# Kernel tuning notes

Hardware: AMD Instinct MI355X
Metric: run time of the kernel (lower is better)

## Reference

```python
import jax, jax.numpy as jnp
import numpy as np
import math

B, L, D, H, FACTOR = 4, 2048, 256, 8, 5
DH = D // H

def setup_inputs() -> dict:
    key = jax.random.key(0)
    ks = jax.random.split(key, 12)
    s = 1.0 / math.sqrt(D)
    return {
        "q": jax.random.normal(ks[0], (B, L, D), jnp.float32),
        "k": jax.random.normal(ks[1], (B, L, D), jnp.float32),
        "v": jax.random.normal(ks[2], (B, L, D), jnp.float32),
        "Wq": jax.random.normal(ks[3], (D, D), jnp.float32) * s,
        "bq": jax.random.normal(ks[4], (D,), jnp.float32) * s,
        "Wk": jax.random.normal(ks[5], (D, D), jnp.float32) * s,
        "bk": jax.random.normal(ks[6], (D,), jnp.float32) * s,
        "Wv": jax.random.normal(ks[7], (D, D), jnp.float32) * s,
        "bv": jax.random.normal(ks[8], (D,), jnp.float32) * s,
        "Wc": jax.random.normal(ks[9], (D, D), jnp.float32) * s,
        "bc": jax.random.normal(ks[10], (D,), jnp.float32) * s,
        "index_sample": jax.random.randint(ks[11], (L,), 0, L),  # U_part = min(5*L*ceil(log1p(L)), L) = L
    }

def reference(q, k, v, Wq, bq, Wk, bk, Wv, bv, Wc, bc, index_sample):
    # projections (torch Linear: x @ W^T + b)
    qp = q @ Wq.T + bq
    kp = k @ Wk.T + bk
    vp = v @ Wv.T + bv
    # NOTE: original reshapes q with a raw view (no transpose), k/v via split()
    q4 = qp.reshape(B, H, L, DH)                       # faithful to q.view(B, H, L, dh)
    k4 = kp.reshape(B, L, H, DH).transpose(0, 2, 1, 3)
    v4 = vp.reshape(B, L, H, DH).transpose(0, 2, 1, 3)
    qf = q4.reshape(B * H, L, DH)
    kf = k4.reshape(B * H, L, DH)
    vf = v4.reshape(B * H, L, DH)
    # random K sampling (with replacement); U_part == L here
    K_sample = kf[:, index_sample, :]                  # [BH, L, dh]
    QK = jnp.einsum('bld,bud->blu', qf, K_sample)      # [BH, L, L]
    M = QK.max(axis=-1) - QK.sum(axis=-1) / L          # sparsity measure [BH, L]
    u = min(FACTOR * math.ceil(math.log1p(L)), L)      # = 40
    _, top_idx = jax.lax.top_k(-M, u)                  # topk(..., largest=False)
    Q_red = jnp.take_along_axis(qf, top_idx[:, :, None], axis=1)  # [BH, u, dh]
    scores = jnp.einsum('bud,bld->bul', Q_red, kf) / math.sqrt(DH)
    probs = jax.nn.softmax(scores, axis=-1)
    out = jnp.einsum('bul,bld->bud', probs, vf)        # [BH, u, dh]
    out = out.reshape(B, H, u, DH).transpose(0, 2, 1, 3).reshape(B, u, D)
    return out @ Wc.T + bc
```

## Files before the change

### kernel.cpp

```cpp
#include <hip/hip_runtime.h>
#include <math.h>

#define B_ 4
#define L_ 2048
#define D_ 256
#define H_ 8
#define DH_ 32
#define NH_ 32
#define U_ 40
#define LD_ 524288
#define NCH_ 16

typedef __attribute__((ext_vector_type(8))) short short8;
typedef __attribute__((ext_vector_type(4))) float floatx4;

static __device__ __forceinline__ unsigned long long ullmin_(unsigned long long a, unsigned long long b) {
    return a < b ? a : b;
}
static __device__ __forceinline__ unsigned short f2bf_rne(float x) {
    unsigned u = __float_as_uint(x);
    unsigned r = u + 0x7FFFu + ((u >> 16) & 1u);
    return (unsigned short)(r >> 16);
}
static __device__ __forceinline__ float bf2f(unsigned short h) {
    return __uint_as_float(((unsigned)h) << 16);
}

__global__ __launch_bounds__(256) void gemm_mfma3(const float* __restrict__ q,
                                                  const float* __restrict__ k,
                                                  const float* __restrict__ v,
                                                  const float* __restrict__ Wq,
                                                  const float* __restrict__ Wk,
                                                  const float* __restrict__ Wv,
                                                  const float* __restrict__ bq,
                                                  const float* __restrict__ bk,
                                                  const float* __restrict__ bv,
                                                  float* __restrict__ qp,
                                                  float* __restrict__ kp,
                                                  float* __restrict__ vp) {
    const int mat = blockIdx.z;
    const float* X = (mat == 0) ? q : (mat == 1) ? k : v;
    const float* W = (mat == 0) ? Wq : (mat == 1) ? Wk : Wv;
    const float* bias = (mat == 0) ? bq : (mat == 1) ? bk : bv;
    float* Y = (mat == 0) ? qp : (mat == 1) ? kp : vp;

    const int t = threadIdx.x;
    const int w = t >> 6, lane = t & 63;
    const int lq = lane & 15, quad = lane >> 4;
    const int colBase = blockIdx.y * 64;
    const int rowBaseW = blockIdx.x * 128 + w * 32;

    __shared__ unsigned short Bls[24576];

    floatx4 acc[2][4];
#pragma unroll
    for (int mt = 0; mt < 2; ++mt)
#pragma unroll
        for (int nt = 0; nt < 4; ++nt) acc[mt][nt] = (floatx4){0.f, 0.f, 0.f, 0.f};

    for (int phase = 0; phase < 2; ++phase) {
        __syncthreads();
#pragma unroll
        for (int r = 0; r < 8; ++r) {
            const int e = t + 256 * r;
            const int col = e >> 5;
            const int k4u = e & 31;
            const int kk = phase * 128 + k4u * 4;
            const float4 x = *(const float4*)(W + (size_t)(colBase + col) * 256 + kk);
            float xs[4] = {x.x, x.y, x.z, x.w};
            unsigned short hv[4], mv4[4], lv[4];
#pragma unroll
            for (int j = 0; j < 4; ++j) {
                hv[j] = f2bf_rne(xs[j]);
                const float e1 = xs[j] - bf2f(hv[j]);
                mv4[j] = f2bf_rne(e1);
                const float e2 = e1 - bf2f(mv4[j]);
                lv[j] = f2bf_rne(e2);
            }
            const int nt = col >> 4, cin = col & 15;
            const int ktl = k4u >> 3, kin = (k4u & 7) * 4;
            const int base = nt * 512 + cin * 32 + kin;
            *(ushort4*)&Bls[((0 * 4 + ktl) << 11) + base] = make_ushort4(hv[0], hv[1], hv[2], hv[3]);
            *(ushort4*)&Bls[((1 * 4 + ktl) << 11) + base] = make_ushort4(mv4[0], mv4[1], mv4[2], mv4[3]);
            *(ushort4*)&Bls[((2 * 4 + ktl) << 11) + base] = make_ushort4(lv[0], lv[1], lv[2], lv[3]);
        }
        __syncthreads();

#pragma unroll
        for (int ktl = 0; ktl < 4; ++ktl) {
            const int kt = phase * 4 + ktl;
            short8 Bh[4], Bm[4], Bl[4];
            const int fo = lq * 32 + quad * 8;
#pragma unroll
            for (int j = 0; j < 4; ++j) {
                Bh[j] = *(const short8*)&Bls[((0 * 4 + ktl) << 11) + j * 512 + fo];
                Bm[j] = *(const short8*)&Bls[((1 * 4 + ktl) << 11) + j * 512 + fo];
                Bl[j] = *(const short8*)&Bls[((2 * 4 + ktl) << 11) + j * 512 + fo];
            }
#pragma unroll
            for (int mt = 0; mt < 2; ++mt) {
                const int m = rowBaseW + mt * 16 + lq;
                short8 Ah, Am, Al;
                {
                    const float* xr = X + (size_t)m * 256 + kt * 32 + quad * 8;
                    const float4 x0 = *(const float4*)xr;
                    const float4 x1 = *(const float4*)(xr + 4);
                    float xs[8] = {x0.x, x0.y, x0.z, x0.w, x1.x, x1.y, x1.z, x1.w};
#pragma unroll
                    for (int j = 0; j < 8; ++j) {
                        const unsigned short h = f2bf_rne(xs[j]);
                        const float e1 = xs[j] - bf2f(h);
                        const unsigned short md = f2bf_rne(e1);
                        const float e2 = e1 - bf2f(md);
                        Ah[j] = (short)h;
                        Am[j] = (short)md;
                        Al[j] = (short)f2bf_rne(e2);
                    }
                }
#pragma unroll
                for (int j = 0; j < 4; ++j) {
                    floatx4 a = acc[mt][j];
                    a = __builtin_amdgcn_mfma_f32_16x16x32_bf16(Am, Bm[j], a, 0, 0, 0);
                    a = __builtin_amdgcn_mfma_f32_16x16x32_bf16(Ah, Bl[j], a, 0, 0, 0);
                    a = __builtin_amdgcn_mfma_f32_16x16x32_bf16(Al, Bh[j], a, 0, 0, 0);
                    a = __builtin_amdgcn_mfma_f32_16x16x32_bf16(Ah, Bm[j], a, 0, 0, 0);
                    a = __builtin_amdgcn_mfma_f32_16x16x32_bf16(Am, Bh[j], a, 0, 0, 0);
                    a = __builtin_amdgcn_mfma_f32_16x16x32_bf16(Ah, Bh[j], a, 0, 0, 0);
                    acc[mt][j] = a;
                }
            }
        }
    }

#pragma unroll
    for (int mt = 0; mt < 2; ++mt)
#pragma unroll
        for (int nt = 0; nt < 4; ++nt) {
            const int c = colBase + nt * 16 + lq;
            const float bv_ = bias[c];
#pragma unroll
            for (int r = 0; r < 4; ++r) {
                const int mr = rowBaseW + mt * 16 + quad * 4 + r;
                Y[(size_t)mr * 256 + c] = acc[mt][nt][r] + bv_;
            }
        }
}

__global__ __launch_bounds__(256) void gemm_out(const float* __restrict__ X,
                                                const float* __restrict__ Wc,
                                                const float* __restrict__ bias,
                                                float* __restrict__ Y) {
    const int t = threadIdx.x;
    const int rowBase = blockIdx.x * 16;
    const int colBase = blockIdx.y * 64;
    const int col = colBase + (t & 63);
    const int rq = (t >> 6) * 4;

    __shared__ float Xs[16][256];
#pragma unroll
    for (int e = t; e < 1024; e += 256) {
        const int r = e >> 6, kq = (e & 63) * 4;
        *(float4*)&Xs[r][kq] = *(const float4*)(X + (size_t)(rowBase + r) * 256 + kq);
    }
    __syncthreads();

    const float* wr = Wc + (size_t)col * 256;
    float acc[4] = {0.f, 0.f, 0.f, 0.f};
#pragma unroll 8
    for (int k = 0; k < 256; k += 4) {
        const float4 wv = *(const float4*)(wr + k);
#pragma unroll
        for (int r = 0; r < 4; ++r) {
            acc[r] = fmaf(Xs[rq + r][k + 0], wv.x, acc[r]);
            acc[r] = fmaf(Xs[rq + r][k + 1], wv.y, acc[r]);
            acc[r] = fmaf(Xs[rq + r][k + 2], wv.z, acc[r]);
            acc[r] = fmaf(Xs[rq + r][k + 3], wv.w, acc[r]);
        }
    }

    const float bv = bias[col];
#pragma unroll
    for (int r = 0; r < 4; ++r)
        Y[(size_t)(rowBase + rq + r) * 256 + col] = acc[r] + bv;
}

__global__ __launch_bounds__(256) void kconv_ksum(const float* __restrict__ kp,
                                                  const int* __restrict__ idx,
                                                  unsigned short* __restrict__ Khi,
                                                  unsigned short* __restrict__ Klo,
                                                  float* __restrict__ Ksum32) {
    const int blk = blockIdx.x;
    const int i = blk >> 5, uc = blk & 31;
    const int b = i >> 3, h = i & 7;
    const int t = threadIdx.x;
    const int dq = (t & 7) * 4;
    const int ur = t >> 3;

    __shared__ float part[32][36];
    float ksum[4] = {0.f, 0.f, 0.f, 0.f};

#pragma unroll
    for (int p = 0; p < 2; ++p) {
        int u = uc * 64 + p * 32 + ur;
        const float4 x = *(const float4*)(kp + (size_t)b * LD_ + (size_t)idx[u] * D_ + h * DH_ + dq);
        float xs[4] = {x.x, x.y, x.z, x.w};
        unsigned short hv[4], lv[4];
#pragma unroll
        for (int j = 0; j < 4; ++j) {
            ksum[j] += xs[j];
            hv[j] = f2bf_rne(xs[j]);
            lv[j] = f2bf_rne(xs[j] - bf2f(hv[j]));
        }
        size_t o = ((size_t)i * 2048 + u) * 32 + dq;
        *(ushort4*)(Khi + o) = make_ushort4(hv[0], hv[1], hv[2], hv[3]);
        *(ushort4*)(Klo + o) = make_ushort4(lv[0], lv[1], lv[2], lv[3]);
    }
#pragma unroll
    for (int j = 0; j < 4; ++j) part[ur][dq + j] = ksum[j];
    __syncthreads();
    if (t < 32) {
        float s = 0.f;
#pragma unroll 8
        for (int u2 = 0; u2 < 32; ++u2) s += part[u2][t];
        Ksum32[(size_t)blk * 32 + t] = s;
    }
}

__global__ __launch_bounds__(256) void mpart_mfma(const float* __restrict__ qp,
                                                  const unsigned short* __restrict__ Khi,
                                                  const unsigned short* __restrict__ Klo,
                                                  const float* __restrict__ Ksum32,
                                                  float* __restrict__ Mv,
                                                  float* __restrict__ Qmean) {
    const int blk = blockIdx.x;
    const int i = blk >> 5;
    const int lg = blk & 31;
    const int t = threadIdx.x;
    const int w = t >> 6;
    const int lane = t & 63;
    const int lq = lane & 15;
    const int quad = lane >> 4;

    __shared__ float ssum[32];
    __shared__ float red[4][64];
    if (t < 32) {
        float s = 0.f;
#pragma unroll 8
        for (int uc = 0; uc < 32; ++uc) s += Ksum32[((size_t)i * 32 + uc) * 32 + t];
        ssum[t] = s;
    }

    short8 Ah[4], Al[4];
#pragma unroll
    for (int lt = 0; lt < 4; ++lt) {
        const int l = lg * 64 + lt * 16 + lq;
        const float* qrow = qp + ((size_t)i * 2048 + l) * 32 + quad * 8;
        float4 x0 = *(const float4*)(qrow);
        float4 x1 = *(const float4*)(qrow + 4);
        float xs[8] = {x0.x, x0.y, x0.z, x0.w, x1.x, x1.y, x1.z, x1.w};
#pragma unroll
        for (int j = 0; j < 8; ++j) {
            unsigned short h = f2bf_rne(xs[j]);
            unsigned short lo = f2bf_rne(xs[j] - bf2f(h));
            Ah[lt][j] = (short)h;
            Al[lt][j] = (short)lo;
        }
    }

    floatx4 rmax[4];
#pragma unroll
    for (int lt = 0; lt < 4; ++lt)
        rmax[lt] = (floatx4){-INFINITY, -INFINITY, -INFINITY, -INFINITY};

    const size_t kfrag = ((size_t)i * 2048 + w * 512 + lq) * 32 + quad * 8;
    const unsigned short* ph = Khi + kfrag;
    const unsigned short* pl = Klo + kfrag;
#pragma unroll 2
    for (int s = 0; s < 32; ++s) {
        short8 Bh = *(const short8*)(ph + (size_t)s * 512);
        short8 Bl = *(const short8*)(pl + (size_t)s * 512);
#pragma unroll
        for (int lt = 0; lt < 4; ++lt) {
            floatx4 acc = (floatx4){0.f, 0.f, 0.f, 0.f};
            acc = __builtin_amdgcn_mfma_f32_16x16x32_bf16(Al[lt], Bh, acc, 0, 0, 0);
            acc = __builtin_amdgcn_mfma_f32_16x16x32_bf16(Ah[lt], Bl, acc, 0, 0, 0);
            acc = __builtin_amdgcn_mfma_f32_16x16x32_bf16(Ah[lt], Bh, acc, 0, 0, 0);
#pragma unroll
            for (int r = 0; r < 4; ++r) rmax[lt][r] = fmaxf(rmax[lt][r], acc[r]);
        }
    }

#pragma unroll
    for (int lt = 0; lt < 4; ++lt)
#pragma unroll
        for (int r = 0; r < 4; ++r) {
            float v = rmax[lt][r];
#pragma unroll
            for (int off = 1; off < 16; off <<= 1)
                v = fmaxf(v, __shfl_xor(v, off, 64));
            rmax[lt][r] = v;
        }
    if (lq == 0) {
#pragma unroll
        for (int lt = 0; lt < 4; ++lt)
#pragma unroll
            for (int r = 0; r < 4; ++r)
                red[w][lt * 16 + quad * 4 + r] = rmax[lt][r];
    }
    __syncthreads();
    if (t < 64) {
        const int l = lg * 64 + t;
        float m = fmaxf(fmaxf(red[0][t], red[1][t]), fmaxf(red[2][t], red[3][t]));
        const float4* q4 = (const float4*)(qp + ((size_t)i * 2048 + l) * 32);
        const float4* s4 = (const float4*)ssum;
        float qs = 0.f;
#pragma unroll
        for (int z = 0; z < 8; ++z) {
            float4 a = q4[z];
            float4 c = s4[z];
            qs = fmaf(a.x, c.x, qs);
            qs = fmaf(a.y, c.y, qs);
            qs = fmaf(a.z, c.z, qs);
            qs = fmaf(a.w, c.w, qs);
        }
        const float qm = qs * (1.0f / 2048.0f);
        Qmean[(size_t)i * 2048 + l] = qm;
        Mv[(size_t)i * 2048 + l] = m - qm;
    }
}

__global__ __launch_bounds__(256) void topk64_kernel(const float* __restrict__ Mv,
                                                     int* __restrict__ candIdx) {
    const int i = blockIdx.x;
    const int t = threadIdx.x;
    unsigned long long keys[8];
    __shared__ unsigned long long wred[4];
#pragma unroll
    for (int j = 0; j < 8; ++j) {
        const int l = t + 256 * j;
        unsigned u32 = __float_as_uint(Mv[(size_t)i * 2048 + l]);
        u32 = (u32 & 0x80000000u) ? ~u32 : (u32 | 0x80000000u);
        keys[j] = ((unsigned long long)u32 << 32) | (unsigned)l;
    }
    for (int it = 0; it < 64; ++it) {
        unsigned long long best = keys[0];
#pragma unroll
        for (int j = 1; j < 8; ++j) best = ullmin_(best, keys[j]);
#pragma unroll
        for (int off = 1; off < 64; off <<= 1)
            best = ullmin_(best, __shfl_xor(best, off, 64));
        if ((t & 63) == 0) wred[t >> 6] = best;
        __syncthreads();
        const unsigned long long m = ullmin_(ullmin_(wred[0], wred[1]), ullmin_(wred[2], wred[3]));
        if (t == 0) candIdx[i * 64 + it] = (int)(m & 0xffffffffu);
#pragma unroll
        for (int j = 0; j < 8; ++j)
            if (keys[j] == m) keys[j] = ~0ULL;
        __syncthreads();
    }
}

__global__ __launch_bounds__(256) void refine_kernel(const float* __restrict__ qp,
                                                     const float* __restrict__ kp,
                                                     const int* __restrict__ idx,
                                                     const int* __restrict__ candIdx,
                                                     float* __restrict__ refPart) {
    const int blk = blockIdx.x;
    const int i = blk >> 3, c = blk & 7;
    const int b = i >> 3, h = i & 7;
    const int t = threadIdx.x;
    __shared__ float qc[64][40];
    __shared__ float Ks[128][40];

    {
        const int cand = t >> 2, dp = (t & 3) * 8;
        const int l = candIdx[i * 64 + cand];
        const float* src = qp + ((size_t)i * 2048 + l) * 32 + dp;
        *(float4*)&qc[cand][dp] = *(const float4*)(src);
        *(float4*)&qc[cand][dp + 4] = *(const float4*)(src + 4);
    }
    __syncthreads();

    const int cand = t >> 2, usub = t & 3;
    float qv[32];
#pragma unroll
    for (int z = 0; z < 8; ++z) {
        float4 a = *(const float4*)&qc[cand][z * 4];
        qv[4 * z] = a.x; qv[4 * z + 1] = a.y; qv[4 * z + 2] = a.z; qv[4 * z + 3] = a.w;
    }

    float m = -INFINITY;
    for (int s = 0; s < 2; ++s) {
        {
            const int r = t >> 1, half = t & 1;
            const int u = c * 256 + s * 128 + r;
            const float* krow = kp + (size_t)b * LD_ + (size_t)idx[u] * D_ + h * DH_ + half * 16;
#pragma unroll
            for (int z = 0; z < 4; ++z)
                *(float4*)&Ks[r][half * 16 + z * 4] = *(const float4*)(krow + z * 4);
        }
        __syncthreads();
        for (int ur = usub; ur < 128; ur += 4) {
            float a0 = 0, a1 = 0, a2 = 0, a3 = 0;
#pragma unroll
            for (int z = 0; z < 8; ++z) {
                float4 kv = *(const float4*)&Ks[ur][z * 4];
                a0 = fmaf(qv[4 * z], kv.x, a0);
                a1 = fmaf(qv[4 * z + 1], kv.y, a1);
                a2 = fmaf(qv[4 * z + 2], kv.z, a2);
                a3 = fmaf(qv[4 * z + 3], kv.w, a3);
            }
            m = fmaxf(m, (a0 + a1) + (a2 + a3));
        }
        __syncthreads();
    }
    m = fmaxf(m, __shfl_xor(m, 1, 64));
    m = fmaxf(m, __shfl_xor(m, 2, 64));
    if ((t & 3) == 0) refPart[((size_t)i * 8 + c) * 64 + cand] = m;
}

__global__ __launch_bounds__(64) void select40_kernel(const int* __restrict__ candIdx,
                                                      const float* __restrict__ refPart,
                                                      const float* __restrict__ Qmean,
                                                      int* __restrict__ topIdx) {
    const int i = blockIdx.x;
    const int t = threadIdx.x;
    const int l = candIdx[i * 64 + t];
    float m = -INFINITY;
#pragma unroll
    for (int c = 0; c < 8; ++c) m = fmaxf(m, refPart[((size_t)i * 8 + c) * 64 + t]);
    float Mex = m - Qmean[(size_t)i * 2048 + l];
    unsigned u32 = __float_as_uint(Mex);
    u32 = (u32 & 0x80000000u) ? ~u32 : (u32 | 0x80000000u);
    unsigned long long key = ((unsigned long long)u32 << 32) | (unsigned)l;
    for (int it = 0; it < 40; ++it) {
        unsigned long long k2 = key;
#pragma unroll
        for (int off = 1; off < 64; off <<= 1) k2 = ullmin_(k2, __shfl_xor(k2, off, 64));
        if (key == k2) {
            topIdx[i * 40 + it] = l;
            key = ~0ULL;
        }
    }
}

#define SCP2 136
#define VSP 36

__global__ __launch_bounds__(320) void attn_part(const float* __restrict__ qp,
                                                 const float* __restrict__ kp,
                                                 const float* __restrict__ vp,
                                                 const int* __restrict__ topIdx,
                                                 float* __restrict__ mPart,
                                                 float* __restrict__ sPart,
                                                 float* __restrict__ oPart) {
    const int blk = blockIdx.x;
    const int i = blk >> 4, c = blk & 15;
    const int b = i >> 3, h = i & 7;
    const int t = threadIdx.x;

    __shared__ float Qs[40][32];
    __shared__ float Vs[128][VSP];
    __shared__ float sc[40][SCP2];
    __shared__ float mred[40], sred[40];

    {
        const int r = t >> 3, qq = t & 7;
        const int lq = topIdx[i * 40 + r];
        *(float4*)&Qs[r][qq * 4] = *(const float4*)(qp + ((size_t)i * 2048 + lq) * 32 + qq * 4);
    }
    for (int e = t; e < 1024; e += 320) {
        const int r = e >> 3, qq = e & 7;
        *(float4*)&Vs[r][qq * 4] =
            *(const float4*)(vp + (size_t)b * LD_ + (size_t)(c * 128 + r) * 256 + h * 32 + qq * 4);
    }
    __syncthreads();

    const float scale = 0.17677669529663687f;

    if (t < 256) {
        const int r = t >> 1;
        const int j0 = (t & 1) * 20;
        const float* kr = kp + (size_t)b * LD_ + (size_t)(c * 128 + r) * 256 + h * 32;
        float kv[32];
#pragma unroll
        for (int z = 0; z < 8; ++z) {
            float4 x = *(const float4*)(kr + z * 4);
            kv[4 * z] = x.x; kv[4 * z + 1] = x.y; kv[4 * z + 2] = x.z; kv[4 * z + 3] = x.w;
        }
#pragma unroll 4
        for (int jj = 0; jj < 20; ++jj) {
            const int j = j0 + jj;
            float a0 = 0, a1 = 0, a2 = 0, a3 = 0;
#pragma unroll
            for (int z = 0; z < 8; ++z) {
                const float4 q4 = *(const float4*)&Qs[j][z * 4];
                a0 = fmaf(kv[4 * z], q4.x, a0);
                a1 = fmaf(kv[4 * z + 1], q4.y, a1);
                a2 = fmaf(kv[4 * z + 2], q4.z, a2);
                a3 = fmaf(kv[4 * z + 3], q4.w, a3);
            }
            sc[j][r] = ((a0 + a1) + (a2 + a3)) * scale;
        }
    }
    __syncthreads();

    {
        const int w = t >> 6, lane = t & 63;
#pragma unroll
        for (int rr = 0; rr < 8; ++rr) {
            const int j = w * 8 + rr;
            float x0 = sc[j][lane], x1 = sc[j][lane + 64];
            float m = fmaxf(x0, x1);
#pragma unroll
            for (int off = 1; off < 64; off <<= 1) m = fmaxf(m, __shfl_xor(m, off, 64));
            const float e0 = __expf(x0 - m), e1 = __expf(x1 - m);
            sc[j][lane] = e0; sc[j][lane + 64] = e1;
            float s = e0 + e1;
#pragma unroll
            for (int off = 1; off < 64; off <<= 1) s += __shfl_xor(s, off, 64);
            if (lane == 0) { mred[j] = m; sred[j] = s; }
        }
    }
    __syncthreads();

    {
        const int j = t >> 3, qq = t & 7;
        float4 acc = make_float4(0.f, 0.f, 0.f, 0.f);
        for (int l = 0; l < 128; ++l) {
            const float p = sc[j][l];
            const float4 v4 = *(const float4*)&Vs[l][qq * 4];
            acc.x = fmaf(p, v4.x, acc.x);
            acc.y = fmaf(p, v4.y, acc.y);
            acc.z = fmaf(p, v4.z, acc.z);
            acc.w = fmaf(p, v4.w, acc.w);
        }
        const size_t o = (size_t)(i * NCH_ + c) * 40 + j;
        *(float4*)&oPart[o * 32 + qq * 4] = acc;
        if (qq == 0) { mPart[o] = mred[j]; sPart[o] = sred[j]; }
    }
}

__global__ __launch_bounds__(256) void attn_combine(const float* __restrict__ mPart,
                                                    const float* __restrict__ sPart,
                                                    const float* __restrict__ oPart,
                                                    float* __restrict__ attnOut) {
    const int i = blockIdx.x;
    const int b = i >> 3, h = i & 7;
    const int t = threadIdx.x;
    for (int e = t; e < 1280; e += 256) {
        const int j = e >> 5, d = e & 31;
        float mv[NCH_];
        float M = -INFINITY;
#pragma unroll
        for (int c = 0; c < NCH_; ++c) {
            mv[c] = mPart[(size_t)(i * NCH_ + c) * 40 + j];
            M = fmaxf(M, mv[c]);
        }
        float S = 0.f, O = 0.f;
#pragma unroll
        for (int c = 0; c < NCH_; ++c) {
            const float sc_ = __expf(mv[c] - M);
            const size_t o = (size_t)(i * NCH_ + c) * 40 + j;
            S = fmaf(sPart[o], sc_, S);
            O = fmaf(oPart[o * 32 + d], sc_, O);
        }
        attnOut[((size_t)b * 40 + j) * 256 + h * 32 + d] = O / S;
    }
}

extern "C" void kernel_launch(void* const* d_in, const int* in_sizes, int n_in,
                              void* d_out, int out_size, void* d_ws, size_t ws_size,
                              hipStream_t stream) {
    const float* q  = (const float*)d_in[0];
    const float* k  = (const float*)d_in[1];
    const float* v  = (const float*)d_in[2];
    const float* Wq = (const float*)d_in[3];
    const float* bq = (const float*)d_in[4];
    const float* Wk = (const float*)d_in[5];
    const float* bk = (const float*)d_in[6];
    const float* Wv = (const float*)d_in[7];
    const float* bv = (const float*)d_in[8];
    const float* Wc = (const float*)d_in[9];
    const float* bc = (const float*)d_in[10];
    const int* idx  = (const int*)d_in[11];
    float* out = (float*)d_out;

    char* w = (char*)d_ws;
    float*          qp      = (float*)(w);
    float*          kp      = (float*)(w + (8u << 20));
    float*          vp      = (float*)(w + (16u << 20));
    unsigned short* Khi     = (unsigned short*)(w + (24u << 20));
    unsigned short* Klo     = (unsigned short*)(w + (28u << 20));
    float*          Mv      = (float*)(w + (32u << 20));
    float*          Qmean   = (float*)(w + (32u << 20) + (256u << 10));
    float*          Ksum32  = (float*)(w + (32u << 20) + (512u << 10));
    int*            candIdx = (int*)  (w + (32u << 20) + (640u << 10));
    int*            topIdx  = (int*)  (w + (32u << 20) + (648u << 10));
    float*          refPart = (float*)(w + (32u << 20) + (656u << 10));
    float*          attnOut = (float*)(w + (32u << 20) + (720u << 10));
    float*          mPart   = (float*)(w + (24u << 20));
    float*          sPart   = (float*)(w + (24u << 20) + (128u << 10));
    float*          oPart   = (float*)(w + (24u << 20) + (256u << 10));

    hipLaunchKernelGGL(gemm_mfma3, dim3(64, 4, 3), dim3(256), 0, stream,
                       q, k, v, Wq, Wk, Wv, bq, bk, bv, qp, kp, vp);
    hipLaunchKernelGGL(kconv_ksum, dim3(1024), dim3(256), 0, stream, kp, idx, Khi, Klo, Ksum32);
    hipLaunchKernelGGL(mpart_mfma, dim3(1024), dim3(256), 0, stream, qp, Khi, Klo, Ksum32, Mv, Qmean);
    hipLaunchKernelGGL(topk64_kernel, dim3(32), dim3(256), 0, stream, Mv, candIdx);
    hipLaunchKernelGGL(refine_kernel, dim3(256), dim3(256), 0, stream, qp, kp, idx, candIdx, refPart);
    hipLaunchKernelGGL(select40_kernel, dim3(32), dim3(64), 0, stream, candIdx, refPart, Qmean, topIdx);
    hipLaunchKernelGGL(attn_part, dim3(512), dim3(320), 0, stream, qp, kp, vp, topIdx, mPart, sPart, oPart);
    hipLaunchKernelGGL(attn_combine, dim3(32), dim3(256), 0, stream, mPart, sPart, oPart, attnOut);
    hipLaunchKernelGGL(gemm_out, dim3(10, 4), dim3(256), 0, stream, attnOut, Wc, bc, out);
}
```

Measured before the change: 247.5 us.

## Fuse small tail kernels: topk into refine, select into attn, combine into output GEMM

Merges the tail of the pipeline from six launches into three. Top-64 candidate selection is recomputed redundantly inside each of the 8 refine blocks per head. The 40-way selection now runs at the start of every attention-partial block, overlapped with V tile loading. The partial-softmax combine is folded into the output projection GEMM. This removes launch gaps and intermediate global round-trips, at the cost of duplicated top-k and select work in each block.

After: 269.9 us. +9.1%, slower.

```diff
diff --git a/kernel.cpp b/kernel.cpp
--- a/kernel.cpp
+++ b/kernel.cpp
@@ -146,44 +146,6 @@
         }
 }
 
-__global__ __launch_bounds__(256) void gemm_out(const float* __restrict__ X,
-                                                const float* __restrict__ Wc,
-                                                const float* __restrict__ bias,
-                                                float* __restrict__ Y) {
-    const int t = threadIdx.x;
-    const int rowBase = blockIdx.x * 16;
-    const int colBase = blockIdx.y * 64;
-    const int col = colBase + (t & 63);
-    const int rq = (t >> 6) * 4;
-
-    __shared__ float Xs[16][256];
-#pragma unroll
-    for (int e = t; e < 1024; e += 256) {
-        const int r = e >> 6, kq = (e & 63) * 4;
-        *(float4*)&Xs[r][kq] = *(const float4*)(X + (size_t)(rowBase + r) * 256 + kq);
-    }
-    __syncthreads();
-
-    const float* wr = Wc + (size_t)col * 256;
-    float acc[4] = {0.f, 0.f, 0.f, 0.f};
-#pragma unroll 8
-    for (int k = 0; k < 256; k += 4) {
-        const float4 wv = *(const float4*)(wr + k);
-#pragma unroll
-        for (int r = 0; r < 4; ++r) {
-            acc[r] = fmaf(Xs[rq + r][k + 0], wv.x, acc[r]);
-            acc[r] = fmaf(Xs[rq + r][k + 1], wv.y, acc[r]);
-            acc[r] = fmaf(Xs[rq + r][k + 2], wv.z, acc[r]);
-            acc[r] = fmaf(Xs[rq + r][k + 3], wv.w, acc[r]);
-        }
-    }
-
-    const float bv = bias[col];
-#pragma unroll
-    for (int r = 0; r < 4; ++r)
-        Y[(size_t)(rowBase + rq + r) * 256 + col] = acc[r] + bv;
-}
-
 __global__ __launch_bounds__(256) void kconv_ksum(const float* __restrict__ kp,
                                                   const int* __restrict__ idx,
                                                   unsigned short* __restrict__ Khi,
@@ -329,12 +291,23 @@
     }
 }
 
-__global__ __launch_bounds__(256) void topk64_kernel(const float* __restrict__ Mv,
-                                                     int* __restrict__ candIdx) {
-    const int i = blockIdx.x;
+__global__ __launch_bounds__(256) void topk_refine(const float* __restrict__ Mv,
+                                                   const float* __restrict__ qp,
+                                                   const float* __restrict__ kp,
+                                                   const int* __restrict__ idx,
+                                                   int* __restrict__ candIdx,
+                                                   float* __restrict__ refPart) {
+    const int blk = blockIdx.x;
+    const int i = blk >> 3, c = blk & 7;
+    const int b = i >> 3, h = i & 7;
     const int t = threadIdx.x;
+
+    __shared__ unsigned long long wred[4];
+    __shared__ int candLds[64];
+    __shared__ float qc[64][40];
+    __shared__ float Ks[128][40];
+
     unsigned long long keys[8];
-    __shared__ unsigned long long wred[4];
 #pragma unroll
     for (int j = 0; j < 8; ++j) {
         const int l = t + 256 * j;
@@ -352,29 +325,17 @@
         if ((t & 63) == 0) wred[t >> 6] = best;
         __syncthreads();
         const unsigned long long m = ullmin_(ullmin_(wred[0], wred[1]), ullmin_(wred[2], wred[3]));
-        if (t == 0) candIdx[i * 64 + it] = (int)(m & 0xffffffffu);
+        if (t == 0) candLds[it] = (int)(m & 0xffffffffu);
 #pragma unroll
         for (int j = 0; j < 8; ++j)
             if (keys[j] == m) keys[j] = ~0ULL;
         __syncthreads();
     }
-}
-
-__global__ __launch_bounds__(256) void refine_kernel(const float* __restrict__ qp,
-                                                     const float* __restrict__ kp,
-                                                     const int* __restrict__ idx,
-                                                     const int* __restrict__ candIdx,
-                                                     float* __restrict__ refPart) {
-    const int blk = blockIdx.x;
-    const int i = blk >> 3, c = blk & 7;
-    const int b = i >> 3, h = i & 7;
-    const int t = threadIdx.x;
-    __shared__ float qc[64][40];
-    __shared__ float Ks[128][40];
+    if (c == 0 && t < 64) candIdx[i * 64 + t] = candLds[t];
 
     {
         const int cand = t >> 2, dp = (t & 3) * 8;
-        const int l = candIdx[i * 64 + cand];
+        const int l = candLds[cand];
         const float* src = qp + ((size_t)i * 2048 + l) * 32 + dp;
         *(float4*)&qc[cand][dp] = *(const float4*)(src);
         *(float4*)&qc[cand][dp + 4] = *(const float4*)(src + 4);
@@ -419,38 +380,15 @@
     if ((t & 3) == 0) refPart[((size_t)i * 8 + c) * 64 + cand] = m;
 }
 
-__global__ __launch_bounds__(64) void select40_kernel(const int* __restrict__ candIdx,
-                                                      const float* __restrict__ refPart,
-                                                      const float* __restrict__ Qmean,
-                                                      int* __restrict__ topIdx) {
-    const int i = blockIdx.x;
-    const int t = threadIdx.x;
-    const int l = candIdx[i * 64 + t];
-    float m = -INFINITY;
-#pragma unroll
-    for (int c = 0; c < 8; ++c) m = fmaxf(m, refPart[((size_t)i * 8 + c) * 64 + t]);
-    float Mex = m - Qmean[(size_t)i * 2048 + l];
-    unsigned u32 = __float_as_uint(Mex);
-    u32 = (u32 & 0x80000000u) ? ~u32 : (u32 | 0x80000000u);
-    unsigned long long key = ((unsigned long long)u32 << 32) | (unsigned)l;
-    for (int it = 0; it < 40; ++it) {
-        unsigned long long k2 = key;
-#pragma unroll
-        for (int off = 1; off < 64; off <<= 1) k2 = ullmin_(k2, __shfl_xor(k2, off, 64));
-        if (key == k2) {
-            topIdx[i * 40 + it] = l;
-            key = ~0ULL;
-        }
-    }
-}
-
 #define SCP2 136
 #define VSP 36
 
 __global__ __launch_bounds__(320) void attn_part(const float* __restrict__ qp,
                                                  const float* __restrict__ kp,
                                                  const float* __restrict__ vp,
-                                                 const int* __restrict__ topIdx,
+                                                 const int* __restrict__ candIdx,
+                                                 const float* __restrict__ refPart,
+                                                 const float* __restrict__ Qmean,
                                                  float* __restrict__ mPart,
                                                  float* __restrict__ sPart,
                                                  float* __restrict__ oPart) {
@@ -463,16 +401,39 @@
     __shared__ float Vs[128][VSP];
     __shared__ float sc[40][SCP2];
     __shared__ float mred[40], sred[40];
+    __shared__ int topl[40];
+
+    if (t < 64) {
+        const int l = candIdx[i * 64 + t];
+        float m = -INFINITY;
+#pragma unroll
+        for (int cc = 0; cc < 8; ++cc) m = fmaxf(m, refPart[((size_t)i * 8 + cc) * 64 + t]);
+        float Mex = m - Qmean[(size_t)i * 2048 + l];
+        unsigned u32 = __float_as_uint(Mex);
+        u32 = (u32 & 0x80000000u) ? ~u32 : (u32 | 0x80000000u);
+        unsigned long long key = ((unsigned long long)u32 << 32) | (unsigned)l;
+        for (int it = 0; it < 40; ++it) {
+            unsigned long long k2 = key;
+#pragma unroll
+            for (int off = 1; off < 64; off <<= 1) k2 = ullmin_(k2, __shfl_xor(k2, off, 64));
+            if (key == k2) {
+                topl[it] = l;
+                key = ~0ULL;
+            }
+        }
+    } else {
+        for (int e = t - 64; e < 1024; e += 256) {
+            const int r = e >> 3, qq = e & 7;
+            *(float4*)&Vs[r][qq * 4] =
+                *(const float4*)(vp + (size_t)b * LD_ + (size_t)(c * 128 + r) * 256 + h * 32 + qq * 4);
+        }
+    }
+    __syncthreads();
 
     {
         const int r = t >> 3, qq = t & 7;
-        const int lq = topIdx[i * 40 + r];
+        const int lq = topl[r];
         *(float4*)&Qs[r][qq * 4] = *(const float4*)(qp + ((size_t)i * 2048 + lq) * 32 + qq * 4);
-    }
-    for (int e = t; e < 1024; e += 320) {
-        const int r = e >> 3, qq = e & 7;
-        *(float4*)&Vs[r][qq * 4] =
-            *(const float4*)(vp + (size_t)b * LD_ + (size_t)(c * 128 + r) * 256 + h * 32 + qq * 4);
     }
     __syncthreads();
 
@@ -541,15 +502,25 @@
     }
 }
 
-__global__ __launch_bounds__(256) void attn_combine(const float* __restrict__ mPart,
+__global__ __launch_bounds__(256) void combine_gemm(const float* __restrict__ mPart,
                                                     const float* __restrict__ sPart,
                                                     const float* __restrict__ oPart,
-                                                    float* __restrict__ attnOut) {
-    const int i = blockIdx.x;
-    const int b = i >> 3, h = i & 7;
+                                                    const float* __restrict__ Wc,
+                                                    const float* __restrict__ bias,
+                                                    float* __restrict__ Y) {
     const int t = threadIdx.x;
-    for (int e = t; e < 1280; e += 256) {
-        const int j = e >> 5, d = e & 31;
+    const int rowBase = blockIdx.x * 16;
+    const int colBase = blockIdx.y * 64;
+
+    __shared__ float Xs[16][256];
+    __shared__ float scl[128][17];
+    __shared__ float Sv[128];
+
+    if (t < 128) {
+        const int r16 = t >> 3, h = t & 7;
+        const int row = rowBase + r16;
+        const int b = row / 40, j = row - b * 40;
+        const int i = b * 8 + h;
         float mv[NCH_];
         float M = -INFINITY;
 #pragma unroll
@@ -557,16 +528,52 @@
             mv[c] = mPart[(size_t)(i * NCH_ + c) * 40 + j];
             M = fmaxf(M, mv[c]);
         }
-        float S = 0.f, O = 0.f;
+        float S = 0.f;
 #pragma unroll
         for (int c = 0; c < NCH_; ++c) {
             const float sc_ = __expf(mv[c] - M);
-            const size_t o = (size_t)(i * NCH_ + c) * 40 + j;
-            S = fmaf(sPart[o], sc_, S);
-            O = fmaf(oPart[o * 32 + d], sc_, O);
-        }
-        attnOut[((size_t)b * 40 + j) * 256 + h * 32 + d] = O / S;
-    }
+            scl[t][c] = sc_;
+            S = fmaf(sPart[(size_t)(i * NCH_ + c) * 40 + j], sc_, S);
+        }
+        Sv[t] = S;
+    }
+    __syncthreads();
+
+    for (int e = t; e < 4096; e += 256) {
+        const int r16 = e >> 8, rem = e & 255;
+        const int h = rem >> 5, d = rem & 31;
+        const int p = r16 * 8 + h;
+        const int row = rowBase + r16;
+        const int b = row / 40, j = row - b * 40;
+        const int i = b * 8 + h;
+        float O = 0.f;
+#pragma unroll
+        for (int c = 0; c < NCH_; ++c)
+            O = fmaf(oPart[((size_t)(i * NCH_ + c) * 40 + j) * 32 + d], scl[p][c], O);
+        Xs[r16][h * 32 + d] = O / Sv[p];
+    }
+    __syncthreads();
+
+    const int col = colBase + (t & 63);
+    const int rq = (t >> 6) * 4;
+    const float* wr = Wc + (size_t)col * 256;
+    float acc[4] = {0.f, 0.f, 0.f, 0.f};
+#pragma unroll 8
+    for (int k = 0; k < 256; k += 4) {
+        const float4 wv = *(const float4*)(wr + k);
+#pragma unroll
+        for (int r = 0; r < 4; ++r) {
+            acc[r] = fmaf(Xs[rq + r][k + 0], wv.x, acc[r]);
+            acc[r] = fmaf(Xs[rq + r][k + 1], wv.y, acc[r]);
+            acc[r] = fmaf(Xs[rq + r][k + 2], wv.z, acc[r]);
+            acc[r] = fmaf(Xs[rq + r][k + 3], wv.w, acc[r]);
+        }
+    }
+
+    const float bv = bias[col];
+#pragma unroll
+    for (int r = 0; r < 4; ++r)
+        Y[(size_t)(rowBase + rq + r) * 256 + col] = acc[r] + bv;
 }
 
 extern "C" void kernel_launch(void* const* d_in, const int* in_sizes, int n_in,
@@ -596,9 +603,7 @@
     float*          Qmean   = (float*)(w + (32u << 20) + (256u << 10));
     float*          Ksum32  = (float*)(w + (32u << 20) + (512u << 10));
     int*            candIdx = (int*)  (w + (32u << 20) + (640u << 10));
-    int*            topIdx  = (int*)  (w + (32u << 20) + (648u << 10));
     float*          refPart = (float*)(w + (32u << 20) + (656u << 10));
-    float*          attnOut = (float*)(w + (32u << 20) + (720u << 10));
     float*          mPart   = (float*)(w + (24u << 20));
     float*          sPart   = (float*)(w + (24u << 20) + (128u << 10));
     float*          oPart   = (float*)(w + (24u << 20) + (256u << 10));
@@ -607,10 +612,9 @@
                        q, k, v, Wq, Wk, Wv, bq, bk, bv, qp, kp, vp);
     hipLaunchKernelGGL(kconv_ksum, dim3(1024), dim3(256), 0, stream, kp, idx, Khi, Klo, Ksum32);
     hipLaunchKernelGGL(mpart_mfma, dim3(1024), dim3(256), 0, stream, qp, Khi, Klo, Ksum32, Mv, Qmean);
-    hipLaunchKernelGGL(topk64_kernel, dim3(32), dim3(256), 0, stream, Mv, candIdx);
-    hipLaunchKernelGGL(refine_kernel, dim3(256), dim3(256), 0, stream, qp, kp, idx, candIdx, refPart);
-    hipLaunchKernelGGL(select40_kernel, dim3(32), dim3(64), 0, stream, candIdx, refPart, Qmean, topIdx);
-    hipLaunchKernelGGL(attn_part, dim3(512), dim3(320), 0, stream, qp, kp, vp, topIdx, mPart, sPart, oPart);
-    hipLaunchKernelGGL(attn_combine, dim3(32), dim3(256), 0, stream, mPart, sPart, oPart, attnOut);
-    hipLaunchKernelGGL(gemm_out, dim3(10, 4), dim3(256), 0, stream, attnOut, Wc, bc, out);
-}
+    hipLaunchKernelGGL(topk_refine, dim3(256), dim3(256), 0, stream, Mv, qp, kp, idx, candIdx, refPart);
+    hipLaunchKernelGGL(attn_part, dim3(512), dim3(320), 0, stream,
+                       qp, kp, vp, candIdx, refPart, Qmean, mPart, sPart, oPart);
+    hipLaunchKernelGGL(combine_gemm, dim3(10, 4), dim3(256), 0, stream,
+                       mPart, sPart, oPart, Wc, bc, out);
+}
```
